# Optimization experiments

Measured on AMD Instinct MI355X. Metric: run time of the kernel, lower is better.

Reference implementation:

```python
import jax, jax.numpy as jnp
import numpy as np
from jax import lax

HIDDEN = 512

def _rnn_layer(xs, W_ih, W_hh, b):
    # xs: [B,T,F] -> ys: [B,T,H]; h_t = tanh(x_t W_ih^T + b + h_{t-1} W_hh^T)
    B = xs.shape[0]
    xp = jnp.einsum('btf,hf->bth', xs, W_ih) + b  # precompute input projections
    def step(h, xp_t):
        h = jnp.tanh(xp_t + h @ W_hh.T)
        return h, h
    h0 = jnp.zeros((B, W_hh.shape[0]), dtype=xs.dtype)
    _, ys = lax.scan(step, h0, xp.transpose(1, 0, 2))  # scan over time
    return ys.transpose(1, 0, 2)


def setup_inputs() -> dict:
    key = jax.random.key(0)
    ks = jax.random.split(key, 16)
    B, T, F, H, M, C = 128, 1024, 24, HIDDEN, 1024, 8
    s = 0.05  # small init to keep tanh unsaturated
    inp = {
        'x': jax.random.normal(ks[0], (B, T, F), jnp.float32),
        'W_ih0': jax.random.normal(ks[1], (H, F), jnp.float32) * s,
        'W_hh0': jax.random.normal(ks[2], (H, H), jnp.float32) * s,
        'b_ih0': jnp.zeros((H,), jnp.float32),
        'b_hh0': jnp.zeros((H,), jnp.float32),
        'W_ih1': jax.random.normal(ks[3], (H, H), jnp.float32) * s,
        'W_hh1': jax.random.normal(ks[4], (H, H), jnp.float32) * s,
        'b_ih1': jnp.zeros((H,), jnp.float32),
        'b_hh1': jnp.zeros((H,), jnp.float32),
        'W_ih2': jax.random.normal(ks[5], (H, H), jnp.float32) * s,
        'W_hh2': jax.random.normal(ks[6], (H, H), jnp.float32) * s,
        'b_ih2': jnp.zeros((H,), jnp.float32),
        'b_hh2': jnp.zeros((H,), jnp.float32),
        'W1': jax.random.normal(ks[7], (M, H), jnp.float32) * s,
        'b1': jnp.zeros((M,), jnp.float32),
        'W2': jax.random.normal(ks[8], (C, M), jnp.float32) * s,
        'b2': jnp.zeros((C,), jnp.float32),
    }
    return inp


def reference(x, W_ih0, W_hh0, b_ih0, b_hh0, W_ih1, W_hh1, b_ih1, b_hh1,
              W_ih2, W_hh2, b_ih2, b_hh2, W1, b1, W2, b2):
    h = _rnn_layer(x, W_ih0, W_hh0, b_ih0 + b_hh0)
    h = _rnn_layer(h, W_ih1, W_hh1, b_ih1 + b_hh1)
    h = _rnn_layer(h, W_ih2, W_hh2, b_ih2 + b_hh2)
    last = h[:, -1, :]  # [B,H] last timestep of top layer
    z = last @ W1.T + b1
    z = jax.nn.silu(z)
    return z @ W2.T + b2
```

## Files before the change

### kernel.cpp

```cpp
#include <hip/hip_runtime.h>
#include <cstdint>
#include <cstddef>


typedef _Float16 half_t;
typedef __attribute__((ext_vector_type(2))) _Float16 half2_t;
typedef __attribute__((ext_vector_type(8))) _Float16 frag8;
typedef __attribute__((ext_vector_type(4))) float    frag4;

union U32H2 { unsigned u; half2_t h2; };

__device__ __forceinline__ float dot2(unsigned a, unsigned b, float c) {
#if __has_builtin(__builtin_amdgcn_fdot2)
    U32H2 ua; ua.u = a; U32H2 ub; ub.u = b;
    return __builtin_amdgcn_fdot2(ua.h2, ub.h2, c, false);
#else
    U32H2 ua; ua.u = a; U32H2 ub; ub.u = b;
    c += (float)ua.h2.x * (float)ub.h2.x;
    c += (float)ua.h2.y * (float)ub.h2.y;
    return c;
#endif
}

__device__ __forceinline__ float fast_tanh(float x) {
    float ax = __builtin_fabsf(x);
    float e  = __expf(-2.f * ax);
    float r  = (1.f - e) / (1.f + e);
    return __builtin_copysignf(r, x);
}

#define WN (512 * 512)

__global__ __launch_bounds__(256) void k_cvt(
    const float* whh0, const float* whh1, const float* whh2,
    const float* wih1, const float* wih2,
    const float* bi0, const float* bh0, const float* bi1, const float* bh1,
    const float* bi2, const float* bh2,
    half_t* w16, float* bias)
{
    int idx = blockIdx.x * 256 + threadIdx.x;
    if (idx < 5 * WN) {
        int seg = idx / WN, off = idx % WN;
        const float* s = seg == 0 ? whh0 : seg == 1 ? whh1 : seg == 2 ? whh2
                       : seg == 3 ? wih1 : wih2;
        w16[idx] = (half_t)s[off];
    } else {
        int j = idx - 5 * WN;
        if (j < 3 * 512) {
            int l = j >> 9, o = j & 511;
            const float* a = l == 0 ? bi0 : l == 1 ? bi1 : bi2;
            const float* c = l == 0 ? bh0 : l == 1 ? bh1 : bh2;
            bias[j] = a[o] + c[o];
        }
    }
}

__global__ __launch_bounds__(256) void k_xp0(
    const float* __restrict__ x, const float* __restrict__ wih0,
    const float* __restrict__ bias0, half_t* __restrict__ P)
{
    __shared__ float wl[512 * 24];
    __shared__ float xl[32 * 25];
    int tid = threadIdx.x;
    int r0  = blockIdx.x * 32;
    for (int i = tid; i < 512 * 24; i += 256) wl[i] = wih0[i];
    for (int i = tid; i < 32 * 24; i += 256) {
        int r = i / 24, f = i % 24;
        xl[r * 25 + f] = x[(size_t)(r0 + r) * 24 + f];
    }
    __syncthreads();
    int r = tid >> 3, c = tid & 7;
    float xr[24];
#pragma unroll
    for (int f = 0; f < 24; f++) xr[f] = xl[r * 25 + f];
    size_t orow = (size_t)(r0 + r) * 512;
    for (int og = 0; og < 8; og++) {
        half_t hv[8];
#pragma unroll
        for (int oj = 0; oj < 8; oj++) {
            int o = og * 64 + c * 8 + oj;
            float acc = bias0[o];
#pragma unroll
            for (int f = 0; f < 24; f++) acc = fmaf(xr[f], wl[o * 24 + f], acc);
            hv[oj] = (half_t)acc;
        }
        *(uint4*)(P + orow + og * 64 + c * 8) = *(const uint4*)hv;
    }
}

__global__ __launch_bounds__(512, 2) void k_scan(
    half_t* __restrict__ P, const half_t* __restrict__ whh)
{
    extern __shared__ char smem[];
    uint4*    wl4  = (uint4*)smem;
    unsigned* hbuf = (unsigned*)(smem + 65536);

    int o = threadIdx.x;
    int b = blockIdx.x;
    int sw = o & 7;

    const uint4* wrow = (const uint4*)(whh + (size_t)o * 512);
    uint4 wreg[56];
#pragma unroll
    for (int g = 0; g < 56; g++) wreg[g] = wrow[g];
#pragma unroll
    for (int j = 0; j < 8; j++)
        wl4[o * 8 + (j ^ sw)] = wrow[56 + j];
    if (o < 256) { hbuf[o] = 0u; hbuf[256 + o] = 0u; }
    __syncthreads();

    half_t* Pb = P + (size_t)b * 1024 * 512;
    int cur = 0;
    float xp_next = (float)Pb[o];
    for (int t = 0; t < 1024; t++) {
        float acc0 = xp_next, acc1 = 0.f, acc2 = 0.f, acc3 = 0.f;
        int tn = t + 1 < 1024 ? t + 1 : 1023;
        xp_next = (float)Pb[(size_t)tn * 512 + o];

        const uint4* h4 = (const uint4*)(hbuf + cur * 256);
#pragma unroll
        for (int g = 0; g < 56; g++) {
            uint4 hv = h4[g];
            uint4 wv = wreg[g];
            acc0 = dot2(wv.x, hv.x, acc0);
            acc1 = dot2(wv.y, hv.y, acc1);
            acc2 = dot2(wv.z, hv.z, acc2);
            acc3 = dot2(wv.w, hv.w, acc3);
        }
#pragma unroll
        for (int j = 0; j < 8; j++) {
            uint4 hv = h4[56 + j];
            uint4 wv = wl4[o * 8 + (j ^ sw)];
            acc0 = dot2(wv.x, hv.x, acc0);
            acc1 = dot2(wv.y, hv.y, acc1);
            acc2 = dot2(wv.z, hv.z, acc2);
            acc3 = dot2(wv.w, hv.w, acc3);
        }
        float hn = fast_tanh((acc0 + acc1) + (acc2 + acc3));
        half_t hh = (half_t)hn;
        ((half_t*)(hbuf + (cur ^ 1) * 256))[o] = hh;
        Pb[(size_t)t * 512 + o] = hh;
        __syncthreads();
        cur ^= 1;
    }
}

__global__ __launch_bounds__(256, 2) void k_proj(
    half_t* __restrict__ P, const half_t* __restrict__ w16,
    const float* __restrict__ bias)
{
    extern __shared__ char smem[];
    half_t* A = (half_t*)smem;
    const int AS = 520;
    int tid = threadIdx.x;
    size_t r0 = (size_t)blockIdx.x * 64;

    const uint4* Pg = (const uint4*)(P + r0 * 512);
    for (int u = tid; u < 4096; u += 256) {
        uint4 v = Pg[u];
        int row = u >> 6, col = u & 63;
        *(uint4*)(A + row * AS + col * 8) = v;
    }
    __syncthreads();

    int wave = tid >> 6, lane = tid & 63;
    int lm = lane & 15, lq = lane >> 4;

    frag4 acc[4][8];
#pragma unroll
    for (int mt = 0; mt < 4; mt++)
#pragma unroll
        for (int nt = 0; nt < 8; nt++) acc[mt][nt] = (frag4){0.f, 0.f, 0.f, 0.f};

    for (int kb = 0; kb < 16; kb++) {
        int k0 = kb * 32 + lq * 8;
        frag8 af[4];
#pragma unroll
        for (int mt = 0; mt < 4; mt++)
            af[mt] = *(const frag8*)(A + (mt * 16 + lm) * AS + k0);
        frag8 bf[8];
#pragma unroll
        for (int nt = 0; nt < 8; nt++) {
            int n = wave * 128 + nt * 16 + lm;
            bf[nt] = *(const frag8*)(w16 + (size_t)n * 512 + k0);
        }
#pragma unroll
        for (int mt = 0; mt < 4; mt++)
#pragma unroll
            for (int nt = 0; nt < 8; nt++)
                acc[mt][nt] = __builtin_amdgcn_mfma_f32_16x16x32_f16(
                    af[mt], bf[nt], acc[mt][nt], 0, 0, 0);
    }

#pragma unroll
    for (int mt = 0; mt < 4; mt++) {
        int row = mt * 16 + lq * 4;
#pragma unroll
        for (int nt = 0; nt < 8; nt++) {
            int oc = wave * 128 + nt * 16 + lm;
            float bo = bias[oc];
#pragma unroll
            for (int i = 0; i < 4; i++) {
                float v = acc[mt][nt][i] + bo;
                P[(r0 + row + i) * 512 + oc] = (half_t)v;
            }
        }
    }
}

__global__ __launch_bounds__(256) void k_head(
    const half_t* __restrict__ P, const float* __restrict__ W1,
    const float* __restrict__ b1, const float* __restrict__ W2,
    const float* __restrict__ b2, float* __restrict__ out)
{
    __shared__ float lastv[512];
    __shared__ float zl[1024];
    __shared__ float red[8][33];
    int tid = threadIdx.x, b = blockIdx.x;
    const half_t* lr = P + ((size_t)b * 1024 + 1023) * 512;
    lastv[tid]       = (float)lr[tid];
    lastv[tid + 256] = (float)lr[tid + 256];
    __syncthreads();
#pragma unroll
    for (int i = 0; i < 4; i++) {
        int m = tid + 256 * i;
        const float* wr = W1 + (size_t)m * 512;
        float acc = b1[m];
        for (int k = 0; k < 512; k += 4) {
            float4 wv = *(const float4*)(wr + k);
            acc = fmaf(wv.x, lastv[k],     acc);
            acc = fmaf(wv.y, lastv[k + 1], acc);
            acc = fmaf(wv.z, lastv[k + 2], acc);
            acc = fmaf(wv.w, lastv[k + 3], acc);
        }
        zl[m] = acc / (1.f + __expf(-acc));
    }
    __syncthreads();
    int c = tid & 7, mc = tid >> 3;
    float p = 0.f;
#pragma unroll
    for (int j = 0; j < 32; j++) {
        int m = mc * 32 + j;
        p = fmaf(zl[m], W2[c * 1024 + m], p);
    }
    red[c][mc] = p;
    __syncthreads();
    if (tid < 8) {
        float s = b2[tid];
#pragma unroll
        for (int j = 0; j < 32; j++) s += red[tid][j];
        out[b * 8 + tid] = s;
    }
}

extern "C" void kernel_launch(void* const* d_in, const int* in_sizes, int n_in,
                              void* d_out, int out_size, void* d_ws, size_t ws_size,
                              hipStream_t stream)
{
    const float* x    = (const float*)d_in[0];
    const float* wih0 = (const float*)d_in[1];
    const float* whh0 = (const float*)d_in[2];
    const float* bi0  = (const float*)d_in[3];
    const float* bh0  = (const float*)d_in[4];
    const float* wih1 = (const float*)d_in[5];
    const float* whh1 = (const float*)d_in[6];
    const float* bi1  = (const float*)d_in[7];
    const float* bh1  = (const float*)d_in[8];
    const float* wih2 = (const float*)d_in[9];
    const float* whh2 = (const float*)d_in[10];
    const float* bi2  = (const float*)d_in[11];
    const float* bh2  = (const float*)d_in[12];
    const float* W1   = (const float*)d_in[13];
    const float* b1   = (const float*)d_in[14];
    const float* W2   = (const float*)d_in[15];
    const float* b2   = (const float*)d_in[16];
    float* out = (float*)d_out;

    char* ws = (char*)d_ws;
    half_t* P    = (half_t*)ws;
    half_t* W16  = (half_t*)(ws + 134217728);
    float*  bias = (float*)(ws + 134217728 + 2621440);

    hipFuncSetAttribute((const void*)k_scan,
                        hipFuncAttributeMaxDynamicSharedMemorySize, 67584);
    hipFuncSetAttribute((const void*)k_proj,
                        hipFuncAttributeMaxDynamicSharedMemorySize, 66560);

    k_cvt<<<5126, 256, 0, stream>>>(whh0, whh1, whh2, wih1, wih2,
                                    bi0, bh0, bi1, bh1, bi2, bh2, W16, bias);
    k_xp0<<<4096, 256, 0, stream>>>(x, wih0, bias, P);
    k_scan<<<128, 512, 67584, stream>>>(P, W16 + 0 * WN);
    k_proj<<<2048, 256, 66560, stream>>>(P, W16 + 3 * WN, bias + 512);
    k_scan<<<128, 512, 67584, stream>>>(P, W16 + 1 * WN);
    k_proj<<<2048, 256, 66560, stream>>>(P, W16 + 4 * WN, bias + 1024);
    k_scan<<<128, 512, 67584, stream>>>(P, W16 + 2 * WN);
    k_head<<<128, 256, 0, stream>>>(P, W1, b1, W2, b2, out);
}
```

Baseline: 5.572 ms.

## Split each batch's recurrence across two workgroups with global-memory flag exchange

Each batch row's RNN scan now runs on two cooperating workgroups, each owning half of the hidden outputs. Within a workgroup, two threads share a row's dot product over half the K dimension each and combine with a shuffle. Every step, each half publishes its new hidden values as tagged 64-bit words in global memory and spin-waits on the partner's tags before the next step. This doubles the number of CUs working on the serial recurrence and fits all weights in registers without LDS staging, at the cost of a cross-CU handshake through L2 on every timestep. A cooperative launch is used to ensure co-residency of all 256 blocks.

```diff
diff --git a/kernel.cpp b/kernel.cpp
--- a/kernel.cpp
+++ b/kernel.cpp
@@ -9,6 +9,7 @@
 typedef __attribute__((ext_vector_type(4))) float    frag4;
 
 union U32H2 { unsigned u; half2_t h2; };
+union HU16 { _Float16 h; unsigned short u; };
 
 __device__ __forceinline__ float dot2(unsigned a, unsigned b, float c) {
 #if __has_builtin(__builtin_amdgcn_fdot2)
@@ -30,15 +31,18 @@
 }
 
 #define WN (512 * 512)
+#define XPAR_STRIDE (128 * 2 * 256)
+#define XSLOTS (2 * XPAR_STRIDE)
 
 __global__ __launch_bounds__(256) void k_cvt(
     const float* whh0, const float* whh1, const float* whh2,
     const float* wih1, const float* wih2,
     const float* bi0, const float* bh0, const float* bi1, const float* bh1,
     const float* bi2, const float* bh2,
-    half_t* w16, float* bias)
+    half_t* w16, float* bias, unsigned long long* X)
 {
     int idx = blockIdx.x * 256 + threadIdx.x;
+    if (idx < XSLOTS) X[idx] = 0ull;
     if (idx < 5 * WN) {
         int seg = idx / WN, off = idx % WN;
         const float* s = seg == 0 ? whh0 : seg == 1 ? whh1 : seg == 2 ? whh2
@@ -88,60 +92,76 @@
     }
 }
 
-__global__ __launch_bounds__(512, 2) void k_scan(
-    half_t* __restrict__ P, const half_t* __restrict__ whh)
-{
-    extern __shared__ char smem[];
-    uint4*    wl4  = (uint4*)smem;
-    unsigned* hbuf = (unsigned*)(smem + 65536);
-
-    int o = threadIdx.x;
-    int b = blockIdx.x;
-    int sw = o & 7;
-
-    const uint4* wrow = (const uint4*)(whh + (size_t)o * 512);
-    uint4 wreg[56];
-#pragma unroll
-    for (int g = 0; g < 56; g++) wreg[g] = wrow[g];
-#pragma unroll
-    for (int j = 0; j < 8; j++)
-        wl4[o * 8 + (j ^ sw)] = wrow[56 + j];
-    if (o < 256) { hbuf[o] = 0u; hbuf[256 + o] = 0u; }
+__global__ __launch_bounds__(512, 2) void k_scan2(
+    half_t* __restrict__ P, const half_t* __restrict__ whh,
+    unsigned long long* __restrict__ X, int tag_base)
+{
+    __shared__ __align__(16) _Float16 sh[2][512];
+
+    int tid = threadIdx.x;
+    int g   = blockIdx.x;
+    int b   = g & 127, hf = g >> 7;
+    int rl  = tid >> 1;
+    int kh  = tid & 1;
+    int row = hf * 256 + rl;
+
+    const uint4* wrow = (const uint4*)(whh + (size_t)row * 512 + kh * 256);
+    uint4 wreg[32];
+#pragma unroll
+    for (int i = 0; i < 32; i++) wreg[i] = wrow[i];
+
+    sh[0][tid] = (_Float16)0.f;
     __syncthreads();
 
     half_t* Pb = P + (size_t)b * 1024 * 512;
-    int cur = 0;
-    float xp_next = (float)Pb[o];
-    for (int t = 0; t < 1024; t++) {
-        float acc0 = xp_next, acc1 = 0.f, acc2 = 0.f, acc3 = 0.f;
-        int tn = t + 1 < 1024 ? t + 1 : 1023;
-        xp_next = (float)Pb[(size_t)tn * 512 + o];
-
-        const uint4* h4 = (const uint4*)(hbuf + cur * 256);
-#pragma unroll
-        for (int g = 0; g < 56; g++) {
-            uint4 hv = h4[g];
-            uint4 wv = wreg[g];
-            acc0 = dot2(wv.x, hv.x, acc0);
-            acc1 = dot2(wv.y, hv.y, acc1);
-            acc2 = dot2(wv.z, hv.z, acc2);
-            acc3 = dot2(wv.w, hv.w, acc3);
-        }
-#pragma unroll
-        for (int j = 0; j < 8; j++) {
-            uint4 hv = h4[56 + j];
-            uint4 wv = wl4[o * 8 + (j ^ sw)];
-            acc0 = dot2(wv.x, hv.x, acc0);
-            acc1 = dot2(wv.y, hv.y, acc1);
-            acc2 = dot2(wv.z, hv.z, acc2);
-            acc3 = dot2(wv.w, hv.w, acc3);
-        }
-        float hn = fast_tanh((acc0 + acc1) + (acc2 + acc3));
-        half_t hh = (half_t)hn;
-        ((half_t*)(hbuf + (cur ^ 1) * 256))[o] = hh;
-        Pb[(size_t)t * 512 + o] = hh;
+    unsigned long long* Xpub  = X + (size_t)(b * 2 + hf) * 256;
+    unsigned long long* Xpoll = X + (size_t)(b * 2 + (1 - hf)) * 256;
+
+    float xp_next = (kh == 0) ? (float)Pb[row] : 0.f;
+
+    for (int t = 0; t < 1024; ++t) {
+        int cur = t & 1, nxt = cur ^ 1;
+        const uint4* h4 = (const uint4*)&sh[cur][kh * 256];
+
+        float a0 = 0.f, a1 = 0.f, a2 = 0.f, a3 = 0.f;
+#pragma unroll
+        for (int i = 0; i < 32; i++) {
+            uint4 hv = h4[i];
+            uint4 wv = wreg[i];
+            a0 = dot2(wv.x, hv.x, a0);
+            a1 = dot2(wv.y, hv.y, a1);
+            a2 = dot2(wv.z, hv.z, a2);
+            a3 = dot2(wv.w, hv.w, a3);
+        }
+        float red = (a0 + a1) + (a2 + a3);
+        red += __shfl_xor(red, 1);
+
+        size_t par = (size_t)(t & 1) * XPAR_STRIDE;
+        if (kh == 0) {
+            float hn = fast_tanh(red + xp_next);
+            half_t hh = (half_t)hn;
+            sh[nxt][row] = hh;
+            Pb[(size_t)t * 512 + row] = hh;
+            HU16 hu; hu.h = hh;
+            unsigned long long pk =
+                ((unsigned long long)(unsigned)(tag_base + t + 1) << 32)
+                | (unsigned long long)hu.u;
+            __hip_atomic_store(&Xpub[par + rl], pk,
+                               __ATOMIC_RELAXED, __HIP_MEMORY_SCOPE_AGENT);
+            int tn = t + 1 < 1024 ? t + 1 : 1023;
+            xp_next = (float)Pb[(size_t)tn * 512 + row];
+        }
+        if (tid < 256 && t < 1023) {
+            unsigned need = (unsigned)(tag_base + t + 1);
+            unsigned long long v;
+            do {
+                v = __hip_atomic_load(&Xpoll[par + tid],
+                                      __ATOMIC_RELAXED, __HIP_MEMORY_SCOPE_AGENT);
+            } while ((unsigned)(v >> 32) < need);
+            HU16 hu; hu.u = (unsigned short)(v & 0xffffull);
+            sh[nxt][(1 - hf) * 256 + tid] = hu.h;
+        }
         __syncthreads();
-        cur ^= 1;
     }
 }
 
@@ -250,6 +270,21 @@
 #pragma unroll
         for (int j = 0; j < 32; j++) s += red[tid][j];
         out[b * 8 + tid] = s;
+    }
+}
+
+static inline void launch_scan(half_t* P, const half_t* whh,
+                               unsigned long long* X, int tag_base,
+                               hipStream_t stream)
+{
+    half_t* Pp = P;
+    const half_t* Wp = whh;
+    unsigned long long* Xp = X;
+    int tb = tag_base;
+    void* args[] = {&Pp, &Wp, &Xp, &tb};
+    if (hipLaunchCooperativeKernel((const void*)k_scan2, dim3(256), dim3(512),
+                                   args, 0u, stream) != hipSuccess) {
+        k_scan2<<<256, 512, 0, stream>>>(Pp, Wp, Xp, tb);
     }
 }
 
@@ -280,19 +315,19 @@
     half_t* P    = (half_t*)ws;
     half_t* W16  = (half_t*)(ws + 134217728);
     float*  bias = (float*)(ws + 134217728 + 2621440);
-
-    hipFuncSetAttribute((const void*)k_scan,
-                        hipFuncAttributeMaxDynamicSharedMemorySize, 67584);
+    unsigned long long* X =
+        (unsigned long long*)(ws + 134217728 + 2621440 + 8192);
+
     hipFuncSetAttribute((const void*)k_proj,
                         hipFuncAttributeMaxDynamicSharedMemorySize, 66560);
 
     k_cvt<<<5126, 256, 0, stream>>>(whh0, whh1, whh2, wih1, wih2,
-                                    bi0, bh0, bi1, bh1, bi2, bh2, W16, bias);
+                                    bi0, bh0, bi1, bh1, bi2, bh2, W16, bias, X);
     k_xp0<<<4096, 256, 0, stream>>>(x, wih0, bias, P);
-    k_scan<<<128, 512, 67584, stream>>>(P, W16 + 0 * WN);
+    launch_scan(P, W16 + 0 * WN, X, 0,    stream);
     k_proj<<<2048, 256, 66560, stream>>>(P, W16 + 3 * WN, bias + 512);
-    k_scan<<<128, 512, 67584, stream>>>(P, W16 + 1 * WN);
+    launch_scan(P, W16 + 1 * WN, X, 1024, stream);
     k_proj<<<2048, 256, 66560, stream>>>(P, W16 + 4 * WN, bias + 1024);
-    k_scan<<<128, 512, 67584, stream>>>(P, W16 + 2 * WN);
+    launch_scan(P, W16 + 2 * WN, X, 2048, stream);
     k_head<<<128, 256, 0, stream>>>(P, W1, b1, W2, b2, out);
 }
```

After: 6.057 ms. 8.7% more time.

## Split recurrent scan across 8 cooperating blocks with MFMA and flag-based exchange

Applied to the files above, without the earlier changes.

Replaces the per-batch-row scan (one block per batch element, dot2 over a 512x512 fp16 W_hh) with 64 blocks. Each block owns 16 batch rows and a 64-column slice of the hidden state and computes its slice with 16x16x32 fp16 MFMAs. Every timestep, each block publishes its h slice to global memory as tagged 64-bit values and spin-waits on the seven peer slices, so the recurrence runs across many CUs and uses matrix cores. The cost is a cross-block global-memory handshake on every step, which relies on all 64 blocks being co-resident to avoid deadlock.

```diff
diff --git a/kernel.cpp b/kernel.cpp
--- a/kernel.cpp
+++ b/kernel.cpp
@@ -8,19 +8,7 @@
 typedef __attribute__((ext_vector_type(8))) _Float16 frag8;
 typedef __attribute__((ext_vector_type(4))) float    frag4;
 
-union U32H2 { unsigned u; half2_t h2; };
-
-__device__ __forceinline__ float dot2(unsigned a, unsigned b, float c) {
-#if __has_builtin(__builtin_amdgcn_fdot2)
-    U32H2 ua; ua.u = a; U32H2 ub; ub.u = b;
-    return __builtin_amdgcn_fdot2(ua.h2, ub.h2, c, false);
-#else
-    U32H2 ua; ua.u = a; U32H2 ub; ub.u = b;
-    c += (float)ua.h2.x * (float)ub.h2.x;
-    c += (float)ua.h2.y * (float)ub.h2.y;
-    return c;
-#endif
-}
+union HU16 { _Float16 h; unsigned short u; };
 
 __device__ __forceinline__ float fast_tanh(float x) {
     float ax = __builtin_fabsf(x);
@@ -29,16 +17,22 @@
     return __builtin_copysignf(r, x);
 }
 
+#define SCAN_BAR() \
+    asm volatile("s_waitcnt lgkmcnt(0)\n\ts_barrier" ::: "memory")
+
 #define WN (512 * 512)
+
+#define XSLOTS (2 * 8 * 8 * 1024)
 
 __global__ __launch_bounds__(256) void k_cvt(
     const float* whh0, const float* whh1, const float* whh2,
     const float* wih1, const float* wih2,
     const float* bi0, const float* bh0, const float* bi1, const float* bh1,
     const float* bi2, const float* bh2,
-    half_t* w16, float* bias)
+    half_t* w16, float* bias, unsigned long long* X)
 {
     int idx = blockIdx.x * 256 + threadIdx.x;
+    if (idx < XSLOTS) X[idx] = 0ull;
     if (idx < 5 * WN) {
         int seg = idx / WN, off = idx % WN;
         const float* s = seg == 0 ? whh0 : seg == 1 ? whh1 : seg == 2 ? whh2
@@ -88,60 +82,123 @@
     }
 }
 
-__global__ __launch_bounds__(512, 2) void k_scan(
-    half_t* __restrict__ P, const half_t* __restrict__ whh)
+__global__ __launch_bounds__(256, 1)
+void k_scan8(half_t* __restrict__ P, const half_t* __restrict__ whh,
+             unsigned long long* __restrict__ X, int tag_base)
 {
     extern __shared__ char smem[];
-    uint4*    wl4  = (uint4*)smem;
-    unsigned* hbuf = (unsigned*)(smem + 65536);
-
-    int o = threadIdx.x;
-    int b = blockIdx.x;
-    int sw = o & 7;
-
-    const uint4* wrow = (const uint4*)(whh + (size_t)o * 512);
-    uint4 wreg[56];
-#pragma unroll
-    for (int g = 0; g < 56; g++) wreg[g] = wrow[g];
-#pragma unroll
-    for (int j = 0; j < 8; j++)
-        wl4[o * 8 + (j ^ sw)] = wrow[56 + j];
-    if (o < 256) { hbuf[o] = 0u; hbuf[256 + o] = 0u; }
-    __syncthreads();
-
-    half_t* Pb = P + (size_t)b * 1024 * 512;
+    half_t* Wl = (half_t*)smem;
+    half_t* hl = (half_t*)(smem + 66560);
+
+    const int tid  = threadIdx.x;
+    const int bid  = blockIdx.x;
+    const int c    = bid & 7;
+    const int s    = bid >> 3;
+    const int b0   = c * 16;
+    const int scol = s * 64;
+
+    const int wave = tid >> 6, lane = tid & 63;
+    const int lm = lane & 15, lq = lane >> 4;
+    const int mycol = wave * 16 + lm;
+
+    {
+        const uint4* Wg = (const uint4*)(whh + (size_t)scol * 512);
+        for (int u = tid; u < 4096; u += 256) {
+            int r = u >> 6, col = u & 63;
+            *(uint4*)(Wl + r * 520 + col * 8) = Wg[(size_t)r * 64 + col];
+        }
+    }
+    for (int i = tid; i < 2 * 16 * 520; i += 256) hl[i] = (_Float16)0.f;
+    __syncthreads();
+
+    frag8 bf[16];
+#pragma unroll
+    for (int kb = 0; kb < 16; kb++)
+        bf[kb] = *(const frag8*)(Wl + mycol * 520 + kb * 32 + lq * 8);
+
+    half_t* prow[4];
+#pragma unroll
+    for (int i = 0; i < 4; i++)
+        prow[i] = P + ((size_t)(b0 + lq * 4 + i) * 1024) * 512 + scol + mycol;
+
+    float xpc[4];
+#pragma unroll
+    for (int i = 0; i < 4; i++) xpc[i] = (float)prow[i][0];
+
+    const int j0 = tid * 4;
+    const int ri = j0 >> 6, cj = j0 & 63;
+
     int cur = 0;
-    float xp_next = (float)Pb[o];
-    for (int t = 0; t < 1024; t++) {
-        float acc0 = xp_next, acc1 = 0.f, acc2 = 0.f, acc3 = 0.f;
+    for (int t = 0; t < 1024; ++t) {
+        half_t* hc = hl + cur * (16 * 520);
+        half_t* hn = hl + (cur ^ 1) * (16 * 520);
         int tn = t + 1 < 1024 ? t + 1 : 1023;
-        xp_next = (float)Pb[(size_t)tn * 512 + o];
-
-        const uint4* h4 = (const uint4*)(hbuf + cur * 256);
-#pragma unroll
-        for (int g = 0; g < 56; g++) {
-            uint4 hv = h4[g];
-            uint4 wv = wreg[g];
-            acc0 = dot2(wv.x, hv.x, acc0);
-            acc1 = dot2(wv.y, hv.y, acc1);
-            acc2 = dot2(wv.z, hv.z, acc2);
-            acc3 = dot2(wv.w, hv.w, acc3);
-        }
-#pragma unroll
-        for (int j = 0; j < 8; j++) {
-            uint4 hv = h4[56 + j];
-            uint4 wv = wl4[o * 8 + (j ^ sw)];
-            acc0 = dot2(wv.x, hv.x, acc0);
-            acc1 = dot2(wv.y, hv.y, acc1);
-            acc2 = dot2(wv.z, hv.z, acc2);
-            acc3 = dot2(wv.w, hv.w, acc3);
-        }
-        float hn = fast_tanh((acc0 + acc1) + (acc2 + acc3));
-        half_t hh = (half_t)hn;
-        ((half_t*)(hbuf + (cur ^ 1) * 256))[o] = hh;
-        Pb[(size_t)t * 512 + o] = hh;
-        __syncthreads();
+
+        float xpn[4];
+#pragma unroll
+        for (int i = 0; i < 4; i++)
+            xpn[i] = (float)prow[i][(size_t)tn * 512];
+
+        frag4 acc0 = {0.f, 0.f, 0.f, 0.f};
+        frag4 acc1 = {0.f, 0.f, 0.f, 0.f};
+#pragma unroll
+        for (int kb = 0; kb < 16; kb += 2) {
+            frag8 af0 = *(const frag8*)(hc + lm * 520 + kb * 32 + lq * 8);
+            frag8 af1 = *(const frag8*)(hc + lm * 520 + (kb + 1) * 32 + lq * 8);
+            acc0 = __builtin_amdgcn_mfma_f32_16x16x32_f16(af0, bf[kb],     acc0, 0, 0, 0);
+            acc1 = __builtin_amdgcn_mfma_f32_16x16x32_f16(af1, bf[kb + 1], acc1, 0, 0, 0);
+        }
+
+        unsigned need = (unsigned)(tag_base + t + 1);
+        unsigned long long* Xpub =
+            X + ((((size_t)(t & 1) * 8 + c) * 8 + s) << 10);
+#pragma unroll
+        for (int i = 0; i < 4; i++) {
+            float hv = fast_tanh(acc0[i] + acc1[i] + xpc[i]);
+            _Float16 hh = (_Float16)hv;
+            HU16 hu; hu.h = hh;
+            unsigned long long pk =
+                ((unsigned long long)need << 32) | (unsigned long long)hu.u;
+            __hip_atomic_store(&Xpub[(lq * 4 + i) * 64 + mycol], pk,
+                               __ATOMIC_RELAXED, __HIP_MEMORY_SCOPE_AGENT);
+            hn[(lq * 4 + i) * 520 + scol + mycol] = hh;
+            prow[i][(size_t)t * 512] = hh;
+        }
+
+        if (t < 1023) {
+            const unsigned long long* Xpar =
+                X + (((size_t)(t & 1) * 8 + c) << 13);
+            unsigned long long v[7][4];
+#pragma unroll
+            for (int pi = 0; pi < 7; pi++) {
+                int peer = pi + (pi >= s ? 1 : 0);
+                const unsigned long long* Xp = Xpar + (peer << 10) + j0;
+#pragma unroll
+                for (int q = 0; q < 4; q++)
+                    v[pi][q] = __hip_atomic_load(&Xp[q],
+                                   __ATOMIC_RELAXED, __HIP_MEMORY_SCOPE_AGENT);
+            }
+#pragma unroll
+            for (int pi = 0; pi < 7; pi++) {
+                int peer = pi + (pi >= s ? 1 : 0);
+                const unsigned long long* Xp = Xpar + (peer << 10) + j0;
+                unsigned short h4[4];
+#pragma unroll
+                for (int q = 0; q < 4; q++) {
+                    unsigned long long vv = v[pi][q];
+                    while ((unsigned)(vv >> 32) < need)
+                        vv = __hip_atomic_load(&Xp[q],
+                                 __ATOMIC_RELAXED, __HIP_MEMORY_SCOPE_AGENT);
+                    h4[q] = (unsigned short)vv;
+                }
+                *(unsigned long long*)(hn + ri * 520 + peer * 64 + cj) =
+                    *(const unsigned long long*)h4;
+            }
+        }
+        SCAN_BAR();
         cur ^= 1;
+#pragma unroll
+        for (int i = 0; i < 4; i++) xpc[i] = xpn[i];
     }
 }
 
@@ -280,19 +337,21 @@
     half_t* P    = (half_t*)ws;
     half_t* W16  = (half_t*)(ws + 134217728);
     float*  bias = (float*)(ws + 134217728 + 2621440);
-
-    hipFuncSetAttribute((const void*)k_scan,
-                        hipFuncAttributeMaxDynamicSharedMemorySize, 67584);
+    unsigned long long* X =
+        (unsigned long long*)(ws + 134217728 + 2621440 + 8192);
+
+    hipFuncSetAttribute((const void*)k_scan8,
+                        hipFuncAttributeMaxDynamicSharedMemorySize, 99840);
     hipFuncSetAttribute((const void*)k_proj,
                         hipFuncAttributeMaxDynamicSharedMemorySize, 66560);
 
     k_cvt<<<5126, 256, 0, stream>>>(whh0, whh1, whh2, wih1, wih2,
-                                    bi0, bh0, bi1, bh1, bi2, bh2, W16, bias);
+                                    bi0, bh0, bi1, bh1, bi2, bh2, W16, bias, X);
     k_xp0<<<4096, 256, 0, stream>>>(x, wih0, bias, P);
-    k_scan<<<128, 512, 67584, stream>>>(P, W16 + 0 * WN);
+    k_scan8<<<64, 256, 99840, stream>>>(P, W16 + 0 * WN, X, 0);
     k_proj<<<2048, 256, 66560, stream>>>(P, W16 + 3 * WN, bias + 512);
-    k_scan<<<128, 512, 67584, stream>>>(P, W16 + 1 * WN);
+    k_scan8<<<64, 256, 99840, stream>>>(P, W16 + 1 * WN, X, 1024);
     k_proj<<<2048, 256, 66560, stream>>>(P, W16 + 4 * WN, bias + 1024);
-    k_scan<<<128, 512, 67584, stream>>>(P, W16 + 2 * WN);
+    k_scan8<<<64, 256, 99840, stream>>>(P, W16 + 2 * WN, X, 2048);
     k_head<<<128, 256, 0, stream>>>(P, W1, b1, W2, b2, out);
 }
```

Measured after the change: 13.54 ms. 2.43x slower.
